# Optimization experiments

Measured on AMD Instinct MI355X. Metric: run time of the kernel, lower is better.

The kernel has to match this reference:

```python
import jax, jax.numpy as jnp
import numpy as np

B, S, D = 2, 2048, 4096
H, KVH, HD = 32, 8, 128
MULT = 0.08838834764831845  # 1/sqrt(head_dim)
MAXV = 30.0                 # tanh soft-cap
ROPE_BASE = 10000.0


def _rope_cos_sin(position_ids, hd=HD, base=ROPE_BASE):
    inv_freq = 1.0 / (base ** (jnp.arange(0, hd, 2, dtype=jnp.float32) / hd))
    freqs = position_ids.astype(jnp.float32)[..., None] * inv_freq  # [B,S,hd/2]
    emb = jnp.concatenate([freqs, freqs], axis=-1)                  # [B,S,hd]
    return jnp.cos(emb), jnp.sin(emb)


def _rotate_half(x):
    half = x.shape[-1] // 2
    return jnp.concatenate([-x[..., half:], x[..., :half]], axis=-1)


def setup_inputs() -> dict:
    key = jax.random.key(0)
    ks = jax.random.split(key, 5)
    hidden_states = jax.random.normal(ks[0], (B, S, D), dtype=jnp.float32)
    position_ids = jnp.broadcast_to(jnp.arange(S, dtype=jnp.int64), (B, S))
    # True = masked (causal upper triangle)
    causal = jnp.triu(jnp.ones((S, S), dtype=bool), k=1)
    attention_mask = jnp.broadcast_to(causal, (B, 1, S, S))
    sc = 0.02
    q_w = jax.random.normal(ks[1], (D, H * HD), dtype=jnp.float32) * sc
    k_w = jax.random.normal(ks[2], (D, KVH * HD), dtype=jnp.float32) * sc
    v_w = jax.random.normal(ks[3], (D, KVH * HD), dtype=jnp.float32) * sc
    o_w = jax.random.normal(ks[4], (H * HD, D), dtype=jnp.float32) * sc
    return {"hidden_states": hidden_states, "position_ids": position_ids,
            "attention_mask": attention_mask, "q_w": q_w, "k_w": k_w,
            "v_w": v_w, "o_w": o_w}


def reference(hidden_states, position_ids, attention_mask, q_w, k_w, v_w, o_w):
    bsz, q_len, _ = hidden_states.shape
    q = (hidden_states @ q_w).reshape(bsz, q_len, H, HD).transpose(0, 2, 1, 3)    # [B,H,S,HD]
    k = (hidden_states @ k_w).reshape(bsz, q_len, KVH, HD).transpose(0, 2, 1, 3)  # [B,KVH,S,HD]
    v = (hidden_states @ v_w).reshape(bsz, q_len, KVH, HD).transpose(0, 2, 1, 3)

    cos, sin = _rope_cos_sin(position_ids)   # [B,S,HD]
    cos = cos[:, None]                       # [B,1,S,HD]
    sin = sin[:, None]
    q = q * cos + _rotate_half(q) * sin
    k = k * cos + _rotate_half(k) * sin

    groups = H // KVH
    k = jnp.repeat(k, groups, axis=1)        # [B,H,S,HD]
    v = jnp.repeat(v, groups, axis=1)

    scores = jnp.einsum('bhqd,bhkd->bhqk', q, k).astype(jnp.float32) * MULT
    scores = MAXV * jnp.tanh(scores / MAXV)
    scores = jnp.where(attention_mask, jnp.float32(-10000.0), scores)
    attn = jax.nn.softmax(scores, axis=-1).astype(q.dtype)

    out = jnp.einsum('bhqk,bhkd->bhqd', attn, v)       # [B,H,S,HD]
    out = out.transpose(0, 2, 1, 3).reshape(bsz, q_len, H * HD)
    return out @ o_w
```

## Files before the change

### kernel.cpp

```cpp
#include <hip/hip_runtime.h>
#include <stdint.h>

#define B_ 2
#define S_ 2048
#define D_ 4096
#define H_ 32
#define KVH_ 8
#define HD_ 128
#define GRP_ (H_/KVH_)
#define NQKV 6144
#define MULT_ 0.08838834764831845f
#define MAXV_ 30.0f

typedef __attribute__((ext_vector_type(8))) short s16x8;
typedef __attribute__((ext_vector_type(4))) float fx4;

__device__ __forceinline__ unsigned short f2bf(float f) {
  unsigned int u = __float_as_uint(f);
  u += 0x7fffu + ((u >> 16) & 1u);
  return (unsigned short)(u >> 16);
}
__device__ __forceinline__ float bf2f(unsigned short h) {
  return __uint_as_float(((unsigned int)h) << 16);
}
__device__ __forceinline__ uint32_t pk2(float lo, float hi) {
  return ((uint32_t)f2bf(hi) << 16) | (uint32_t)f2bf(lo);
}

__device__ __forceinline__ void gld_lds16(const void* g, void* l) {
  __builtin_amdgcn_global_load_lds(
      (const __attribute__((address_space(1))) unsigned int*)g,
      (__attribute__((address_space(3))) unsigned int*)l, 16, 0, 0);
}


__global__ void k_f2bf(const float* __restrict__ src, unsigned short* __restrict__ dst, int n4) {
  int i = blockIdx.x * blockDim.x + threadIdx.x;
  int stride = gridDim.x * blockDim.x;
  for (; i < n4; i += stride) {
    float4 v = ((const float4*)src)[i];
    ushort4 o;
    o.x = f2bf(v.x); o.y = f2bf(v.y); o.z = f2bf(v.z); o.w = f2bf(v.w);
    ((ushort4*)dst)[i] = o;
  }
}

__global__ void k_transpose_w(const float* __restrict__ src, int ncols,
                              unsigned short* __restrict__ dst) {
  __shared__ float tile[32][33];
  int k0 = blockIdx.x * 32;
  int n0 = blockIdx.y * 32;
  int tx = threadIdx.x, ty = threadIdx.y;
  for (int i = 0; i < 32; i += 8)
    tile[ty + i][tx] = src[(size_t)(k0 + ty + i) * ncols + n0 + tx];
  __syncthreads();
  for (int i = 0; i < 32; i += 8)
    dst[(size_t)(n0 + ty + i) * 4096 + k0 + tx] = f2bf(tile[tx][ty + i]);
}

__global__ void k_transpose_v(const unsigned short* __restrict__ qkv,
                              unsigned short* __restrict__ vt) {
  __shared__ unsigned short tile[32][33];
  int s0 = blockIdx.x * 32;
  int d0 = blockIdx.y * 32;
  int bk = blockIdx.z;
  int b = bk / KVH_, kvh = bk % KVH_;
  int tx = threadIdx.x, ty = threadIdx.y;
  for (int i = 0; i < 32; i += 8)
    tile[ty + i][tx] = qkv[(size_t)(b*S_ + s0 + ty + i)*NQKV + 5120 + kvh*HD_ + d0 + tx];
  __syncthreads();
  for (int i = 0; i < 32; i += 8)
    vt[((size_t)bk*HD_ + d0 + ty + i)*S_ + s0 + tx] = tile[tx][ty + i];
}

__global__ void k_rope(const unsigned short* __restrict__ qkv,
                       unsigned short* __restrict__ Q, unsigned short* __restrict__ K) {
  int bs = blockIdx.x;
  int b = bs >> 11;
  int s = bs & (S_ - 1);
  __shared__ float cs[64], sn[64];
  int t = threadIdx.x;
  if (t < 64) {
    float inv = __expf(-(float)t * 0.14391156831212787f);
    float fr = (float)s * inv;
    cs[t] = cosf(fr); sn[t] = sinf(fr);
  }
  __syncthreads();
  const unsigned short* row = qkv + (size_t)bs * NQKV;
  for (int i = t; i < H_*HD_; i += 256) {
    int h = i >> 7, d = i & 127;
    float x = bf2f(row[i]);
    float x2, c, si;
    if (d < 64) { x2 = -bf2f(row[h*128 + d + 64]); c = cs[d];    si = sn[d]; }
    else        { x2 =  bf2f(row[h*128 + d - 64]); c = cs[d-64]; si = sn[d-64]; }
    Q[((size_t)(b*H_ + h)*S_ + s)*HD_ + d] = f2bf(x*c + x2*si);
  }
  for (int i = t; i < KVH_*HD_; i += 256) {
    int h = i >> 7, d = i & 127;
    float x = bf2f(row[4096 + i]);
    float x2, c, si;
    if (d < 64) { x2 = -bf2f(row[4096 + h*128 + d + 64]); c = cs[d];    si = sn[d]; }
    else        { x2 =  bf2f(row[4096 + h*128 + d - 64]); c = cs[d-64]; si = sn[d-64]; }
    K[((size_t)(b*KVH_ + h)*S_ + s)*HD_ + d] = f2bf(x*c + x2*si);
  }
}


#define BAR() asm volatile("s_barrier" ::: "memory")
#define VMC4() asm volatile("s_waitcnt vmcnt(4)" ::: "memory")
#define SB0() __builtin_amdgcn_sched_barrier(0)

#define STAGE(buf, isB, h, kt) do {                                          \
  const unsigned short* _src = (isB) ? Bt : A;                               \
  size_t _rb = (size_t)(((isB) ? bn : bm)*256 + (h)*128);                    \
  _Pragma("unroll") for (int _rr = 0; _rr < 2; ++_rr) {                      \
    int _s = _rr*8 + wv;                                                     \
    gld_lds16(_src + (_rb + (size_t)((_s>>1)*16))*Kd                         \
                   + (size_t)((kt)*64 + (_s&1)*32) + lane_off,               \
              ldsc + (buf)*65536 + (isB)*32768 + (h)*16384 + _s*1024);       \
  }                                                                          \
} while (0)

#define LDA(dst, buf, mh) do {                                               \
  _Pragma("unroll") for (int _i = 0; _i < 4; ++_i)                           \
  _Pragma("unroll") for (int _kk = 0; _kk < 2; ++_kk)                        \
    dst[_i*2+_kk] = *(const s16x8*)(ldsc + (buf)*65536 + wr*16384            \
                    + ((((mh)*4+_i)*2+_kk)*1024) + aswz);                    \
} while (0)

#define LDB(dst, buf, nh) do {                                               \
  _Pragma("unroll") for (int _j = 0; _j < 2; ++_j)                           \
  _Pragma("unroll") for (int _kk = 0; _kk < 2; ++_kk)                        \
    dst[_j*2+_kk] = *(const s16x8*)(ldsc + (buf)*65536 + 32768               \
                    + (wc>>1)*16384                                          \
                    + ((((wc&1)*4+(nh)*2+_j)*2+_kk)*1024) + aswz);           \
} while (0)

#define MFMA_Q(Aa, Bb, MH, NH) do {                                          \
  __builtin_amdgcn_s_setprio(1);                                            \
  _Pragma("unroll") for (int _i = 0; _i < 4; ++_i)                           \
  _Pragma("unroll") for (int _j = 0; _j < 2; ++_j)                           \
  _Pragma("unroll") for (int _kk = 0; _kk < 2; ++_kk)                        \
    acc[(MH)*4+_i][(NH)*2+_j] = __builtin_amdgcn_mfma_f32_16x16x32_bf16(     \
        Aa[_i*2+_kk], Bb[_j*2+_kk], acc[(MH)*4+_i][(NH)*2+_j], 0, 0, 0);     \
  __builtin_amdgcn_s_setprio(0);                                            \
} while (0)

template<int OUTF32>
__global__ __launch_bounds__(512, 2)
void k_gemm8(const unsigned short* __restrict__ A, const unsigned short* __restrict__ Bt,
             void* __restrict__ C, int Kdim, int N, int MB) {
  __shared__ __align__(16) char ldsbuf[131072];
  char* ldsc = ldsbuf;
  const size_t Kd = (size_t)Kdim;
  const int NT = Kdim >> 6;

  int nwg = gridDim.x;
  int flat = blockIdx.x;
  int q = nwg >> 3, r8 = nwg & 7, xcd = flat & 7, off = flat >> 3;
  int wg = (xcd < r8 ? xcd*(q+1) : r8*(q+1) + (xcd-r8)*q) + off;
  int bm = wg % MB, bn = wg / MB;

  int tid = threadIdx.x;
  int lane = tid & 63, wv = tid >> 6;
  int wr = wv >> 2, wc = wv & 3;
  int l15 = lane & 15, l4 = lane >> 4;
  const int aswz = (l15 << 6) + ((l4 << 4) ^ ((l15 & 8) ? 32 : 0));
  const size_t lane_off = (size_t)(lane >> 2) * Kd
                        + (size_t)(((lane & 3) << 3) ^ ((lane & 32) >> 1));

  fx4 acc[8][4] = {};
  s16x8 Afr[8], B0fr[4], B1fr[4];

  STAGE(0, 0, 0, 0); STAGE(0, 0, 1, 0);
  STAGE(0, 1, 0, 0); STAGE(0, 1, 1, 0);
  STAGE(1, 1, 0, 1); STAGE(1, 1, 1, 1);
  VMC4();
  BAR();

  for (int t2 = 0; t2 < NT; t2 += 2) {
    int tb1 = t2 + 1;
    int tn0 = t2 + 2; if (tn0 >= NT) tn0 -= NT;
    int tn1 = t2 + 3; if (tn1 >= NT) tn1 -= NT;
    LDA(Afr, 0, 0); LDB(B0fr, 0, 0);
    STAGE(1, 0, 0, tb1);
    BAR();
    MFMA_Q(Afr, B0fr, 0, 0);
    SB0(); BAR();
    LDB(B1fr, 0, 1);
    STAGE(1, 0, 1, tb1);
    BAR();
    MFMA_Q(Afr, B1fr, 0, 1);
    SB0(); BAR();
    LDA(Afr, 0, 1);
    STAGE(0, 1, 0, tn0);
    BAR();
    MFMA_Q(Afr, B1fr, 1, 1);
    SB0(); BAR();
    STAGE(0, 1, 1, tn0);
    BAR();
    MFMA_Q(Afr, B0fr, 1, 0);
    SB0(); VMC4(); BAR();
    LDA(Afr, 1, 0); LDB(B0fr, 1, 0);
    STAGE(0, 0, 0, tn0);
    BAR();
    MFMA_Q(Afr, B0fr, 0, 0);
    SB0(); BAR();
    LDB(B1fr, 1, 1);
    STAGE(0, 0, 1, tn0);
    BAR();
    MFMA_Q(Afr, B1fr, 0, 1);
    SB0(); BAR();
    LDA(Afr, 1, 1);
    STAGE(1, 1, 0, tn1);
    BAR();
    MFMA_Q(Afr, B1fr, 1, 1);
    SB0(); BAR();
    STAGE(1, 1, 1, tn1);
    BAR();
    MFMA_Q(Afr, B0fr, 1, 0);
    SB0(); VMC4(); BAR();
  }

  int m0 = bm*256 + wr*128 + l4*4;
  int n0 = bn*256 + wc*64 + l15;
#pragma unroll
  for (int mf = 0; mf < 8; ++mf)
#pragma unroll
    for (int nf = 0; nf < 4; ++nf)
#pragma unroll
      for (int r = 0; r < 4; ++r) {
        int m = m0 + mf*16 + r;
        int n = n0 + nf*16;
        float v = acc[mf][nf][r];
        if (OUTF32) ((float*)C)[(size_t)m*N + n] = v;
        else ((unsigned short*)C)[(size_t)m*N + n] = f2bf(v);
      }
}


__global__ __launch_bounds__(256)
void k_attn2(const unsigned short* __restrict__ Q, const unsigned short* __restrict__ K,
             const unsigned short* __restrict__ Vt, unsigned short* __restrict__ Aout) {
  __shared__ unsigned short k_lds[32*128];
  __shared__ unsigned short v_lds[128*32];
  const float C1 = 0.08838834764831845f * 2.0f * 1.4426950408889634f / 30.0f;
  const float C2 = 30.0f * 1.4426950408889634f;
  int tpair = blockIdx.x;
  int bh = blockIdx.y;
  int b = bh / H_, h = bh % H_;
  int kvh = h / GRP_;
  int tid = threadIdx.x, lane = tid & 63, wv = tid >> 6;
  int l15 = lane & 15, l4 = lane >> 4;
  const unsigned short* Qb = Q + (size_t)bh * S_ * HD_;
  const unsigned short* Kb = K + (size_t)(b*KVH_ + kvh) * S_ * HD_;
  const unsigned short* Vb = Vt + (size_t)(b*KVH_ + kvh) * HD_ * S_;

  for (int sp = 0; sp < 2; ++sp) {
    int strip = sp ? (15 - tpair) : tpair;
    int q0 = strip * 128;
    int qbase = q0 + wv * 32;
    s16x8 bq[2][4];
#pragma unroll
    for (int qf = 0; qf < 2; ++qf)
#pragma unroll
      for (int kb = 0; kb < 4; ++kb)
        bq[qf][kb] = *(const s16x8*)&Qb[(size_t)(qbase + qf*16 + l15)*HD_ + kb*32 + l4*8];
    fx4 oacc[2][8] = {};
    float sump[2] = {0.f, 0.f};
    int ntiles = q0/32 + 4;
    for (int t = 0; t < ntiles; ++t) {
      int kbase = t*32;
      for (int it = 0; it < 2; ++it) {
        int c = it*256 + tid;
        int kr = c >> 4;
        int kd = ((c & 15) ^ (kr & 7)) * 8;
        gld_lds16(&Kb[(size_t)(kbase + kr)*HD_ + kd], &k_lds[it*2048 + wv*512]);
        int vd = c >> 2;
        int vk = ((c & 3) ^ (vd & 3)) * 8;
        gld_lds16(&Vb[(size_t)vd*S_ + kbase + vk], &v_lds[it*2048 + wv*512]);
      }
      __syncthreads();
      if (kbase <= qbase + 31) {
        fx4 sst[2][2] = {};
#pragma unroll
        for (int nb = 0; nb < 2; ++nb)
#pragma unroll
          for (int kb = 0; kb < 4; ++kb) {
            s16x8 kf = *(const s16x8*)&k_lds[(nb*16 + l15)*128 + (((kb*4 + l4) ^ (l15 & 7)) * 8)];
            sst[nb][0] = __builtin_amdgcn_mfma_f32_16x16x32_bf16(kf, bq[0][kb], sst[nb][0], 0, 0, 0);
            sst[nb][1] = __builtin_amdgcn_mfma_f32_16x16x32_bf16(kf, bq[1][kb], sst[nb][1], 0, 0, 0);
          }
        s16x8 pf[2];
#pragma unroll
        for (int qf = 0; qf < 2; ++qf) {
          int qr = qbase + qf*16 + l15;
          uint32_t w[4];
          float psum = 0.f;
#pragma unroll
          for (int nb = 0; nb < 2; ++nb) {
            float pv[4];
#pragma unroll
            for (int r = 0; r < 4; ++r) {
              int kk = kbase + nb*16 + l4*4 + r;
              float sraw = sst[nb][qf][r];
              float e2 = __builtin_amdgcn_exp2f(-fabsf(sraw) * C1);
              float th = (1.f - e2) * __builtin_amdgcn_rcpf(1.f + e2);
              float th_s = __uint_as_float(__float_as_uint(th) |
                                           (__float_as_uint(sraw) & 0x80000000u));
              float p = __builtin_amdgcn_exp2f(th_s * C2 - C2);
              p = (kk <= qr) ? p : 0.f;
              psum += p;
              pv[r] = p;
            }
            w[nb*2]   = pk2(pv[0], pv[1]);
            w[nb*2+1] = pk2(pv[2], pv[3]);
          }
          sump[qf] += psum;
          uint32_t a0x = __shfl_xor((int)w[0], 16), a1x = __shfl_xor((int)w[1], 16);
          uint32_t b0x = __shfl_xor((int)w[2], 16), b1x = __shfl_xor((int)w[3], 16);
          bool up = (l4 & 1);
          uint32_t VA0 = up ? a0x : w[0], VA1 = up ? a1x : w[1];
          uint32_t VA2 = up ? w[0] : a0x, VA3 = up ? w[1] : a1x;
          uint32_t VB0 = up ? b0x : w[2], VB1 = up ? b1x : w[3];
          uint32_t VB2 = up ? w[2] : b0x, VB3 = up ? w[3] : b1x;
          bool lowh = (l4 < 2);
          uint32_t X0 = lowh ? VB0 : VA0, X1 = lowh ? VB1 : VA1;
          uint32_t X2 = lowh ? VB2 : VA2, X3 = lowh ? VB3 : VA3;
          uint32_t Y0 = __shfl_xor((int)X0, 32), Y1 = __shfl_xor((int)X1, 32);
          uint32_t Y2 = __shfl_xor((int)X2, 32), Y3 = __shfl_xor((int)X3, 32);
          union { uint32_t u[4]; s16x8 v; } tw;
          tw.u[0] = (l4 == 0) ? VA0 : (l4 == 3) ? VB0 : Y0;
          tw.u[1] = (l4 == 0) ? VA1 : (l4 == 3) ? VB1 : Y1;
          tw.u[2] = (l4 == 0) ? VA2 : (l4 == 3) ? VB2 : Y2;
          tw.u[3] = (l4 == 0) ? VA3 : (l4 == 3) ? VB3 : Y3;
          pf[qf] = tw.v;
        }
#pragma unroll
        for (int db = 0; db < 8; ++db) {
          int d = db*16 + l15;
          s16x8 vf = *(const s16x8*)&v_lds[d*32 + ((l4 ^ (d & 3)) * 8)];
          oacc[0][db] = __builtin_amdgcn_mfma_f32_16x16x32_bf16(vf, pf[0], oacc[0][db], 0, 0, 0);
          oacc[1][db] = __builtin_amdgcn_mfma_f32_16x16x32_bf16(vf, pf[1], oacc[1][db], 0, 0, 0);
        }
      }
      __syncthreads();
    }
#pragma unroll
    for (int qf = 0; qf < 2; ++qf) {
      float s = sump[qf];
      s += __shfl_xor(s, 16);
      s += __shfl_xor(s, 32);
      float rn = __builtin_amdgcn_rcpf(s);
      int q = qbase + qf*16 + l15;
#pragma unroll
      for (int db = 0; db < 8; ++db) {
        ushort4 o;
        o.x = f2bf(oacc[qf][db][0] * rn);
        o.y = f2bf(oacc[qf][db][1] * rn);
        o.z = f2bf(oacc[qf][db][2] * rn);
        o.w = f2bf(oacc[qf][db][3] * rn);
        *(ushort4*)&Aout[(size_t)(b*S_ + q)*4096 + h*HD_ + db*16 + l4*4] = o;
      }
    }
  }
}


extern "C" void kernel_launch(void* const* d_in, const int* in_sizes, int n_in,
                              void* d_out, int out_size, void* d_ws, size_t ws_size,
                              hipStream_t stream) {
  (void)in_sizes; (void)n_in; (void)out_size; (void)ws_size;
  const float* hidden = (const float*)d_in[0];
  const float* q_w = (const float*)d_in[3];
  const float* k_w = (const float*)d_in[4];
  const float* v_w = (const float*)d_in[5];
  const float* o_w = (const float*)d_in[6];
  char* ws = (char*)d_ws;
  unsigned short* hidden_bf = (unsigned short*)(ws + 0);
  unsigned short* qkv_wt    = (unsigned short*)(ws + 33554432);
  unsigned short* o_wt      = (unsigned short*)(ws + 83886080);
  unsigned short* qkv       = (unsigned short*)(ws + 117440512);
  unsigned short* Qb        = (unsigned short*)(ws + 167772160);
  unsigned short* Kb        = (unsigned short*)(ws + 201326592);
  unsigned short* Vt        = (unsigned short*)(ws + 209715200);
  unsigned short* attn_out  = (unsigned short*)(ws + 218103808);

  dim3 tb(32, 8);
  k_f2bf<<<2048, 256, 0, stream>>>(hidden, hidden_bf, (B_*S_*D_)/4);
  k_transpose_w<<<dim3(128, 128), tb, 0, stream>>>(q_w, 4096, qkv_wt);
  k_transpose_w<<<dim3(128, 32),  tb, 0, stream>>>(k_w, 1024, qkv_wt + (size_t)4096*4096);
  k_transpose_w<<<dim3(128, 32),  tb, 0, stream>>>(v_w, 1024, qkv_wt + (size_t)5120*4096);
  k_transpose_w<<<dim3(128, 128), tb, 0, stream>>>(o_w, 4096, o_wt);
  k_gemm8<0><<<dim3(16*24), 512, 0, stream>>>(hidden_bf, qkv_wt, qkv, D_, NQKV, 16);
  k_rope<<<B_*S_, 256, 0, stream>>>(qkv, Qb, Kb);
  k_transpose_v<<<dim3(S_/32, HD_/32, B_*KVH_), tb, 0, stream>>>(qkv, Vt);
  k_attn2<<<dim3(8, B_*H_), 256, 0, stream>>>(Qb, Kb, Vt, attn_out);
  k_gemm8<1><<<dim3(16*16), 512, 0, stream>>>(attn_out, o_wt, d_out, D_, D_, 16);
}
```

Before: 595.3 us.

## Double-buffer 64-key KV tiles in attention and parametrize GEMM N-tile

The attention kernel moves from 32-key tiles loaded synchronously to 64-key tiles that are double-buffered in LDS, prefetching the next K/V tile while the current one is computed. MFMA sections are raised in priority with s_setprio. Separately, the GEMM is templated on its N-tile width, and the QKV projection uses a 128-wide N tile over twice as many workgroups to improve CU occupancy across the 6144-wide output. The cost is more LDS per attention block and a more complex causal-skip pattern, since the skip now works at 64-key granularity.

```diff
diff --git a/kernel.cpp b/kernel.cpp
--- a/kernel.cpp
+++ b/kernel.cpp
@@ -107,53 +107,61 @@
 
 
 #define BAR() asm volatile("s_barrier" ::: "memory")
-#define VMC4() asm volatile("s_waitcnt vmcnt(4)" ::: "memory")
 #define SB0() __builtin_amdgcn_sched_barrier(0)
 
 #define STAGE(buf, isB, h, kt) do {                                          \
   const unsigned short* _src = (isB) ? Bt : A;                               \
-  size_t _rb = (size_t)(((isB) ? bn : bm)*256 + (h)*128);                    \
-  _Pragma("unroll") for (int _rr = 0; _rr < 2; ++_rr) {                      \
+  size_t _rb = (size_t)(((isB) ? bn : bm)*((isB) ? BN : 256)                 \
+                        + (h)*((isB) ? BN/2 : 128));                         \
+  _Pragma("unroll") for (int _rr = 0; _rr < ((isB) ? BN/128 : 2); ++_rr) {   \
     int _s = _rr*8 + wv;                                                     \
     gld_lds16(_src + (_rb + (size_t)((_s>>1)*16))*Kd                         \
                    + (size_t)((kt)*64 + (_s&1)*32) + lane_off,               \
-              ldsc + (buf)*65536 + (isB)*32768 + (h)*16384 + _s*1024);       \
+              ldsc + (buf)*PBUF + (isB)*32768                                \
+                   + (h)*((isB) ? BN*64 : 16384) + _s*1024);                 \
   }                                                                          \
 } while (0)
 
 #define LDA(dst, buf, mh) do {                                               \
   _Pragma("unroll") for (int _i = 0; _i < 4; ++_i)                           \
   _Pragma("unroll") for (int _kk = 0; _kk < 2; ++_kk)                        \
-    dst[_i*2+_kk] = *(const s16x8*)(ldsc + (buf)*65536 + wr*16384            \
+    dst[_i*2+_kk] = *(const s16x8*)(ldsc + (buf)*PBUF + wr*16384             \
                     + ((((mh)*4+_i)*2+_kk)*1024) + aswz);                    \
 } while (0)
 
 #define LDB(dst, buf, nh) do {                                               \
-  _Pragma("unroll") for (int _j = 0; _j < 2; ++_j)                           \
+  _Pragma("unroll") for (int _j = 0; _j < NFR; ++_j)                         \
   _Pragma("unroll") for (int _kk = 0; _kk < 2; ++_kk)                        \
-    dst[_j*2+_kk] = *(const s16x8*)(ldsc + (buf)*65536 + 32768               \
-                    + (wc>>1)*16384                                          \
-                    + ((((wc&1)*4+(nh)*2+_j)*2+_kk)*1024) + aswz);           \
+    dst[_j*2+_kk] = *(const s16x8*)(ldsc + (buf)*PBUF + 32768                \
+                    + (wc>>1)*(BN*64)                                        \
+                    + ((((wc&1)*2*NFR+(nh)*NFR+_j)*2+_kk)*1024) + aswz);     \
 } while (0)
 
 #define MFMA_Q(Aa, Bb, MH, NH) do {                                          \
   __builtin_amdgcn_s_setprio(1);                                            \
   _Pragma("unroll") for (int _i = 0; _i < 4; ++_i)                           \
-  _Pragma("unroll") for (int _j = 0; _j < 2; ++_j)                           \
+  _Pragma("unroll") for (int _j = 0; _j < NFR; ++_j)                         \
   _Pragma("unroll") for (int _kk = 0; _kk < 2; ++_kk)                        \
-    acc[(MH)*4+_i][(NH)*2+_j] = __builtin_amdgcn_mfma_f32_16x16x32_bf16(     \
-        Aa[_i*2+_kk], Bb[_j*2+_kk], acc[(MH)*4+_i][(NH)*2+_j], 0, 0, 0);     \
+    acc[(MH)*4+_i][(NH)*NFR+_j] = __builtin_amdgcn_mfma_f32_16x16x32_bf16(   \
+        Aa[_i*2+_kk], Bb[_j*2+_kk], acc[(MH)*4+_i][(NH)*NFR+_j], 0, 0, 0);   \
   __builtin_amdgcn_s_setprio(0);                                            \
 } while (0)
 
-template<int OUTF32>
+template<int OUTF32, int BN>
 __global__ __launch_bounds__(512, 2)
 void k_gemm8(const unsigned short* __restrict__ A, const unsigned short* __restrict__ Bt,
              void* __restrict__ C, int Kdim, int N, int MB) {
-  __shared__ __align__(16) char ldsbuf[131072];
+  constexpr int NFR = BN / 128;
+  constexpr int PBUF = 32768 + BN * 128;
+  __shared__ __align__(16) char ldsbuf[2 * PBUF];
   char* ldsc = ldsbuf;
   const size_t Kd = (size_t)Kdim;
   const int NT = Kdim >> 6;
+
+  auto VMCN = [] {
+    if constexpr (BN == 256) asm volatile("s_waitcnt vmcnt(4)" ::: "memory");
+    else                     asm volatile("s_waitcnt vmcnt(2)" ::: "memory");
+  };
 
   int nwg = gridDim.x;
   int flat = blockIdx.x;
@@ -169,13 +177,13 @@
   const size_t lane_off = (size_t)(lane >> 2) * Kd
                         + (size_t)(((lane & 3) << 3) ^ ((lane & 32) >> 1));
 
-  fx4 acc[8][4] = {};
-  s16x8 Afr[8], B0fr[4], B1fr[4];
+  fx4 acc[8][2*NFR] = {};
+  s16x8 Afr[8], B0fr[2*NFR], B1fr[2*NFR];
 
   STAGE(0, 0, 0, 0); STAGE(0, 0, 1, 0);
   STAGE(0, 1, 0, 0); STAGE(0, 1, 1, 0);
   STAGE(1, 1, 0, 1); STAGE(1, 1, 1, 1);
-  VMC4();
+  VMCN();
   BAR();
 
   for (int t2 = 0; t2 < NT; t2 += 2) {
@@ -200,7 +208,7 @@
     STAGE(0, 1, 1, tn0);
     BAR();
     MFMA_Q(Afr, B0fr, 1, 0);
-    SB0(); VMC4(); BAR();
+    SB0(); VMCN(); BAR();
     LDA(Afr, 1, 0); LDB(B0fr, 1, 0);
     STAGE(0, 0, 0, tn0);
     BAR();
@@ -219,19 +227,18 @@
     STAGE(1, 1, 1, tn1);
     BAR();
     MFMA_Q(Afr, B0fr, 1, 0);
-    SB0(); VMC4(); BAR();
+    SB0(); VMCN(); BAR();
   }
 
   int m0 = bm*256 + wr*128 + l4*4;
-  int n0 = bn*256 + wc*64 + l15;
 #pragma unroll
   for (int mf = 0; mf < 8; ++mf)
 #pragma unroll
-    for (int nf = 0; nf < 4; ++nf)
+    for (int nf = 0; nf < 2*NFR; ++nf)
 #pragma unroll
       for (int r = 0; r < 4; ++r) {
         int m = m0 + mf*16 + r;
-        int n = n0 + nf*16;
+        int n = bn*BN + (wc>>1)*(BN/2) + ((wc&1)*2*NFR + nf)*16 + l15;
         float v = acc[mf][nf][r];
         if (OUTF32) ((float*)C)[(size_t)m*N + n] = v;
         else ((unsigned short*)C)[(size_t)m*N + n] = f2bf(v);
@@ -240,22 +247,36 @@
 
 
 __global__ __launch_bounds__(256)
-void k_attn2(const unsigned short* __restrict__ Q, const unsigned short* __restrict__ K,
+void k_attn3(const unsigned short* __restrict__ Q, const unsigned short* __restrict__ K,
              const unsigned short* __restrict__ Vt, unsigned short* __restrict__ Aout) {
-  __shared__ unsigned short k_lds[32*128];
-  __shared__ unsigned short v_lds[128*32];
+  __shared__ unsigned short k_lds[2][64*128];
+  __shared__ unsigned short v_lds[2][128*64];
   const float C1 = 0.08838834764831845f * 2.0f * 1.4426950408889634f / 30.0f;
   const float C2 = 30.0f * 1.4426950408889634f;
   int tpair = blockIdx.x;
   int bh = blockIdx.y;
-  int b = bh / H_, h = bh % H_;
-  int kvh = h / GRP_;
+  int b = bh >> 5, h = bh & 31;
+  int kvh = h >> 2;
   int tid = threadIdx.x, lane = tid & 63, wv = tid >> 6;
   int l15 = lane & 15, l4 = lane >> 4;
   const unsigned short* Qb = Q + (size_t)bh * S_ * HD_;
   const unsigned short* Kb = K + (size_t)(b*KVH_ + kvh) * S_ * HD_;
   const unsigned short* Vb = Vt + (size_t)(b*KVH_ + kvh) * HD_ * S_;
 
+#define STAGE_KV(bufi, kb64) do {                                            \
+  _Pragma("unroll") for (int _it = 0; _it < 4; ++_it) {                      \
+    int _c = _it*256 + tid;                                                  \
+    int _kr = _c >> 4;                                                       \
+    int _kd = ((_c & 15) ^ (_kr & 7)) * 8;                                   \
+    gld_lds16(&Kb[(size_t)((kb64) + _kr)*HD_ + _kd],                         \
+              &k_lds[bufi][_it*2048 + wv*512]);                              \
+    int _vd = _c >> 3;                                                       \
+    int _vk = ((_c & 7) ^ (_vd & 7)) * 8;                                    \
+    gld_lds16(&Vb[(size_t)_vd*S_ + (kb64) + _vk],                            \
+              &v_lds[bufi][_it*2048 + wv*512]);                              \
+  }                                                                          \
+} while (0)
+
   for (int sp = 0; sp < 2; ++sp) {
     int strip = sp ? (15 - tpair) : tpair;
     int q0 = strip * 128;
@@ -268,81 +289,87 @@
         bq[qf][kb] = *(const s16x8*)&Qb[(size_t)(qbase + qf*16 + l15)*HD_ + kb*32 + l4*8];
     fx4 oacc[2][8] = {};
     float sump[2] = {0.f, 0.f};
-    int ntiles = q0/32 + 4;
-    for (int t = 0; t < ntiles; ++t) {
-      int kbase = t*32;
-      for (int it = 0; it < 2; ++it) {
-        int c = it*256 + tid;
-        int kr = c >> 4;
-        int kd = ((c & 15) ^ (kr & 7)) * 8;
-        gld_lds16(&Kb[(size_t)(kbase + kr)*HD_ + kd], &k_lds[it*2048 + wv*512]);
-        int vd = c >> 2;
-        int vk = ((c & 3) ^ (vd & 3)) * 8;
-        gld_lds16(&Vb[(size_t)vd*S_ + kbase + vk], &v_lds[it*2048 + wv*512]);
-      }
-      __syncthreads();
+    int nt = q0/64 + 2;
+    STAGE_KV(0, 0);
+    __syncthreads();
+    for (int t = 0; t < nt; ++t) {
+      int bufi = t & 1;
+      int kbase = t*64;
+      if (t + 1 < nt) STAGE_KV(bufi^1, (t+1)*64);
       if (kbase <= qbase + 31) {
-        fx4 sst[2][2] = {};
-#pragma unroll
-        for (int nb = 0; nb < 2; ++nb)
+        fx4 sst[4][2] = {};
+        __builtin_amdgcn_s_setprio(1);
+#pragma unroll
+        for (int nb = 0; nb < 4; ++nb)
 #pragma unroll
           for (int kb = 0; kb < 4; ++kb) {
-            s16x8 kf = *(const s16x8*)&k_lds[(nb*16 + l15)*128 + (((kb*4 + l4) ^ (l15 & 7)) * 8)];
+            s16x8 kf = *(const s16x8*)&k_lds[bufi][(nb*16 + l15)*128 +
+                                                   (((kb*4 + l4) ^ (l15 & 7)) * 8)];
             sst[nb][0] = __builtin_amdgcn_mfma_f32_16x16x32_bf16(kf, bq[0][kb], sst[nb][0], 0, 0, 0);
             sst[nb][1] = __builtin_amdgcn_mfma_f32_16x16x32_bf16(kf, bq[1][kb], sst[nb][1], 0, 0, 0);
           }
-        s16x8 pf[2];
+        __builtin_amdgcn_s_setprio(0);
+        s16x8 pf[2][2];
 #pragma unroll
         for (int qf = 0; qf < 2; ++qf) {
           int qr = qbase + qf*16 + l15;
-          uint32_t w[4];
           float psum = 0.f;
 #pragma unroll
-          for (int nb = 0; nb < 2; ++nb) {
-            float pv[4];
-#pragma unroll
-            for (int r = 0; r < 4; ++r) {
-              int kk = kbase + nb*16 + l4*4 + r;
-              float sraw = sst[nb][qf][r];
-              float e2 = __builtin_amdgcn_exp2f(-fabsf(sraw) * C1);
-              float th = (1.f - e2) * __builtin_amdgcn_rcpf(1.f + e2);
-              float th_s = __uint_as_float(__float_as_uint(th) |
-                                           (__float_as_uint(sraw) & 0x80000000u));
-              float p = __builtin_amdgcn_exp2f(th_s * C2 - C2);
-              p = (kk <= qr) ? p : 0.f;
-              psum += p;
-              pv[r] = p;
+          for (int hp = 0; hp < 2; ++hp) {
+            uint32_t w[4];
+#pragma unroll
+            for (int n2 = 0; n2 < 2; ++n2) {
+              int nb = hp*2 + n2;
+              float pv[4];
+#pragma unroll
+              for (int r = 0; r < 4; ++r) {
+                int kk = kbase + nb*16 + l4*4 + r;
+                float sraw = sst[nb][qf][r];
+                float e2 = __builtin_amdgcn_exp2f(-fabsf(sraw) * C1);
+                float th = (1.f - e2) * __builtin_amdgcn_rcpf(1.f + e2);
+                float th_s = __uint_as_float(__float_as_uint(th) |
+                                             (__float_as_uint(sraw) & 0x80000000u));
+                float p = __builtin_amdgcn_exp2f(th_s * C2 - C2);
+                p = (kk <= qr) ? p : 0.f;
+                psum += p;
+                pv[r] = p;
+              }
+              w[n2*2]   = pk2(pv[0], pv[1]);
+              w[n2*2+1] = pk2(pv[2], pv[3]);
             }
-            w[nb*2]   = pk2(pv[0], pv[1]);
-            w[nb*2+1] = pk2(pv[2], pv[3]);
+            uint32_t a0x = __shfl_xor((int)w[0], 16), a1x = __shfl_xor((int)w[1], 16);
+            uint32_t b0x = __shfl_xor((int)w[2], 16), b1x = __shfl_xor((int)w[3], 16);
+            bool up = (l4 & 1);
+            uint32_t VA0 = up ? a0x : w[0], VA1 = up ? a1x : w[1];
+            uint32_t VA2 = up ? w[0] : a0x, VA3 = up ? w[1] : a1x;
+            uint32_t VB0 = up ? b0x : w[2], VB1 = up ? b1x : w[3];
+            uint32_t VB2 = up ? w[2] : b0x, VB3 = up ? w[3] : b1x;
+            bool lowh = (l4 < 2);
+            uint32_t X0 = lowh ? VB0 : VA0, X1 = lowh ? VB1 : VA1;
+            uint32_t X2 = lowh ? VB2 : VA2, X3 = lowh ? VB3 : VA3;
+            uint32_t Y0 = __shfl_xor((int)X0, 32), Y1 = __shfl_xor((int)X1, 32);
+            uint32_t Y2 = __shfl_xor((int)X2, 32), Y3 = __shfl_xor((int)X3, 32);
+            union { uint32_t u[4]; s16x8 v; } tw;
+            tw.u[0] = (l4 == 0) ? VA0 : (l4 == 3) ? VB0 : Y0;
+            tw.u[1] = (l4 == 0) ? VA1 : (l4 == 3) ? VB1 : Y1;
+            tw.u[2] = (l4 == 0) ? VA2 : (l4 == 3) ? VB2 : Y2;
+            tw.u[3] = (l4 == 0) ? VA3 : (l4 == 3) ? VB3 : Y3;
+            pf[qf][hp] = tw.v;
           }
           sump[qf] += psum;
-          uint32_t a0x = __shfl_xor((int)w[0], 16), a1x = __shfl_xor((int)w[1], 16);
-          uint32_t b0x = __shfl_xor((int)w[2], 16), b1x = __shfl_xor((int)w[3], 16);
-          bool up = (l4 & 1);
-          uint32_t VA0 = up ? a0x : w[0], VA1 = up ? a1x : w[1];
-          uint32_t VA2 = up ? w[0] : a0x, VA3 = up ? w[1] : a1x;
-          uint32_t VB0 = up ? b0x : w[2], VB1 = up ? b1x : w[3];
-          uint32_t VB2 = up ? w[2] : b0x, VB3 = up ? w[3] : b1x;
-          bool lowh = (l4 < 2);
-          uint32_t X0 = lowh ? VB0 : VA0, X1 = lowh ? VB1 : VA1;
-          uint32_t X2 = lowh ? VB2 : VA2, X3 = lowh ? VB3 : VA3;
-          uint32_t Y0 = __shfl_xor((int)X0, 32), Y1 = __shfl_xor((int)X1, 32);
-          uint32_t Y2 = __shfl_xor((int)X2, 32), Y3 = __shfl_xor((int)X3, 32);
-          union { uint32_t u[4]; s16x8 v; } tw;
-          tw.u[0] = (l4 == 0) ? VA0 : (l4 == 3) ? VB0 : Y0;
-          tw.u[1] = (l4 == 0) ? VA1 : (l4 == 3) ? VB1 : Y1;
-          tw.u[2] = (l4 == 0) ? VA2 : (l4 == 3) ? VB2 : Y2;
-          tw.u[3] = (l4 == 0) ? VA3 : (l4 == 3) ? VB3 : Y3;
-          pf[qf] = tw.v;
         }
+        __builtin_amdgcn_s_setprio(1);
 #pragma unroll
         for (int db = 0; db < 8; ++db) {
           int d = db*16 + l15;
-          s16x8 vf = *(const s16x8*)&v_lds[d*32 + ((l4 ^ (d & 3)) * 8)];
-          oacc[0][db] = __builtin_amdgcn_mfma_f32_16x16x32_bf16(vf, pf[0], oacc[0][db], 0, 0, 0);
-          oacc[1][db] = __builtin_amdgcn_mfma_f32_16x16x32_bf16(vf, pf[1], oacc[1][db], 0, 0, 0);
+#pragma unroll
+          for (int hp = 0; hp < 2; ++hp) {
+            s16x8 vf = *(const s16x8*)&v_lds[bufi][d*64 + (((hp*4 + l4) ^ (d & 7)) * 8)];
+            oacc[0][db] = __builtin_amdgcn_mfma_f32_16x16x32_bf16(vf, pf[0][hp], oacc[0][db], 0, 0, 0);
+            oacc[1][db] = __builtin_amdgcn_mfma_f32_16x16x32_bf16(vf, pf[1][hp], oacc[1][db], 0, 0, 0);
+          }
         }
+        __builtin_amdgcn_s_setprio(0);
       }
       __syncthreads();
     }
@@ -352,7 +379,7 @@
       s += __shfl_xor(s, 16);
       s += __shfl_xor(s, 32);
       float rn = __builtin_amdgcn_rcpf(s);
-      int q = qbase + qf*16 + l15;
+      int qq = qbase + qf*16 + l15;
 #pragma unroll
       for (int db = 0; db < 8; ++db) {
         ushort4 o;
@@ -360,10 +387,11 @@
         o.y = f2bf(oacc[qf][db][1] * rn);
         o.z = f2bf(oacc[qf][db][2] * rn);
         o.w = f2bf(oacc[qf][db][3] * rn);
-        *(ushort4*)&Aout[(size_t)(b*S_ + q)*4096 + h*HD_ + db*16 + l4*4] = o;
+        *(ushort4*)&Aout[(size_t)(b*S_ + qq)*4096 + h*HD_ + db*16 + l4*4] = o;
       }
     }
   }
+#undef STAGE_KV
 }
 
 
@@ -392,9 +420,9 @@
   k_transpose_w<<<dim3(128, 32),  tb, 0, stream>>>(k_w, 1024, qkv_wt + (size_t)4096*4096);
   k_transpose_w<<<dim3(128, 32),  tb, 0, stream>>>(v_w, 1024, qkv_wt + (size_t)5120*4096);
   k_transpose_w<<<dim3(128, 128), tb, 0, stream>>>(o_w, 4096, o_wt);
-  k_gemm8<0><<<dim3(16*24), 512, 0, stream>>>(hidden_bf, qkv_wt, qkv, D_, NQKV, 16);
+  k_gemm8<0,128><<<dim3(16*48), 512, 0, stream>>>(hidden_bf, qkv_wt, qkv, D_, NQKV, 16);
   k_rope<<<B_*S_, 256, 0, stream>>>(qkv, Qb, Kb);
   k_transpose_v<<<dim3(S_/32, HD_/32, B_*KVH_), tb, 0, stream>>>(qkv, Vt);
-  k_attn2<<<dim3(8, B_*H_), 256, 0, stream>>>(Qb, Kb, Vt, attn_out);
-  k_gemm8<1><<<dim3(16*16), 512, 0, stream>>>(attn_out, o_wt, d_out, D_, D_, 16);
-}
+  k_attn3<<<dim3(8, B_*H_), 256, 0, stream>>>(Qb, Kb, Vt, attn_out);
+  k_gemm8<1,256><<<dim3(16*16), 512, 0, stream>>>(attn_out, o_wt, d_out, D_, D_, 16);
+}
```

Result: slower. 647.5 us (+8.8%).
